# Kernel optimization log

Hardware: AMD Instinct MI355X
Metric: run time of the kernel (lower is better)

The kernel has to match this reference:

```python
import jax, jax.numpy as jnp
import numpy as np

B, S, IN_DIM = 128, 1024, 256
M, D, OUT = 64, 128, 128


def setup_inputs() -> dict:
    key = jax.random.key(0)
    ks = jax.random.split(key, 10)
    def xavier(k, shape):
        fan_in, fan_out = shape[-1], shape[-2] if len(shape) > 1 else shape[-1]
        lim = jnp.sqrt(6.0 / (shape[0] + shape[1]))
        return jax.random.uniform(k, shape, jnp.float32, -lim, lim)
    return {
        "x": jax.random.normal(ks[0], (B, S, IN_DIM), jnp.float32),
        "memory_key": xavier(ks[1], (M, D)),
        "memory_value": xavier(ks[2], (M, D)),
        "Wr": xavier(ks[3], (IN_DIM, D)),
        "br": jnp.zeros((D,), jnp.float32),
        "Ww": xavier(ks[4], (IN_DIM, D)),
        "bw": jnp.zeros((D,), jnp.float32),
        "Wp": xavier(ks[5], (D, OUT)),
        "bp": jnp.zeros((OUT,), jnp.float32),
    }


def reference(x, memory_key, memory_value, Wr, br, Ww, bw, Wp, bp):
    # Precompute time-parallel parts: read keys and write erase/add signals.
    k_all = jnp.einsum("bsi,id->bsd", x, Wr) + br          # [B,S,D]
    v_all = jnp.einsum("bsi,id->bsd", x, Ww) + bw          # [B,S,D]
    erase_all = jax.nn.sigmoid(v_all)                        # [B,S,D]
    add_all = jnp.tanh(v_all)                                # [B,S,D]

    Mv0 = jnp.broadcast_to(memory_value, (x.shape[0],) + memory_value.shape)  # [B,M,D]

    def step(Mv, inp):
        k_t, e_t, a_t = inp                                  # each [B,D]
        w = jax.nn.softmax(k_t @ memory_key.T, axis=-1)      # [B,M]
        r = jnp.einsum("bm,bmd->bd", w, Mv)                # [B,D]
        y = jax.nn.sigmoid(r @ Wp + bp)                      # [B,OUT]
        wE = w[:, :, None]                                   # [B,M,1]
        Mv = Mv * (1.0 - wE * e_t[:, None, :]) + wE * a_t[:, None, :]
        return Mv, y

    xs = (jnp.swapaxes(k_all, 0, 1),
          jnp.swapaxes(erase_all, 0, 1),
          jnp.swapaxes(add_all, 0, 1))                       # [S,B,D] each
    _, ys = jax.lax.scan(step, Mv0, xs)                      # ys: [S,B,OUT]
    return jnp.swapaxes(ys, 0, 1)                            # [B,S,OUT]
```

## Files before the change

### kernel.cpp

```cpp
#include <hip/hip_runtime.h>
#include <hip/hip_bf16.h>


#define B_   128
#define S_   1024
#define IN_  256
#define M_   64
#define D_   128
#define OUT_ 128
#define TC_  4
#define TL_  (S_ / TC_)
#define RC_  (B_ * TL_)

typedef __hip_bfloat16 bf16;
typedef unsigned int uint32;
typedef __attribute__((ext_vector_type(8))) short s16x8;
typedef __attribute__((ext_vector_type(4))) float f32x4;

__device__ __forceinline__ float tof(bf16 v) { return __bfloat162float(v); }
__device__ __forceinline__ bf16  tob(float v) { return __float2bfloat16(v); }
__device__ __forceinline__ float ldf(const float* p, long i) { return p[i]; }
__device__ __forceinline__ float ldf(const bf16* p, long i)  { return tof(p[i]); }
__device__ __forceinline__ void  stf(float* p, long i, float v) { p[i] = v; }
__device__ __forceinline__ void  stf(bf16* p, long i, float v)  { p[i] = tob(v); }
__device__ __forceinline__ void  unp(uint32 u, float& lo, float& hi) {
  lo = __uint_as_float(u << 16);
  hi = __uint_as_float(u & 0xFFFF0000u);
}
__device__ __forceinline__ uint32 pk(float lo, float hi) {
  union { bf16 h; unsigned short u; } a, b;
  a.h = tob(lo); b.h = tob(hi);
  return (uint32)a.u | ((uint32)b.u << 16);
}
__device__ __forceinline__ void split2(float f0, float f1, uint32& h, uint32& l) {
  union { bf16 b; unsigned short u; } a0, a1;
  a0.b = tob(f0); a1.b = tob(f1);
  h = (uint32)a0.u | ((uint32)a1.u << 16);
  const float r0 = f0 - tof(a0.b);
  const float r1 = f1 - tof(a1.b);
  l = pk(r0, r1);
}

__global__ __launch_bounds__(256) void k_probe(const uint32* __restrict__ xw,
                                               int* __restrict__ flag) {
  __shared__ int s[256];
  const int tid = threadIdx.x;
  int sc = 0;
#pragma unroll
  for (int k = 0; k < 8; ++k) {
    const uint32 u = xw[tid * 8 + k];
    const float v = __uint_as_float(u << 16);
    if (!(fabsf(v) < 4.0f)) sc++;
  }
  s[tid] = sc;
  __syncthreads();
  for (int o = 128; o > 0; o >>= 1) {
    if (tid < o) s[tid] += s[tid + o];
    __syncthreads();
  }
  if (tid == 0) *flag = (s[0] > 64) ? 1 : 0;
}

template <typename T>
__device__ void k0_body(const T* Wr, const T* br, const T* K,
                        float* Wk, float* bk) {
  const int idx = blockIdx.x * 256 + threadIdx.x;
  if (idx < IN_ * M_) {
    const int i = idx >> 6, m = idx & 63;
    float acc = 0.f;
    for (int d = 0; d < D_; ++d)
      acc = fmaf(ldf(Wr, (long)i * D_ + d), ldf(K, (long)m * D_ + d), acc);
    Wk[idx] = acc;
  } else if (idx < IN_ * M_ + M_) {
    const int m = idx - IN_ * M_;
    float acc = 0.f;
    for (int d = 0; d < D_; ++d)
      acc = fmaf(ldf(br, d), ldf(K, (long)m * D_ + d), acc);
    bk[m] = acc;
  }
}

__global__ __launch_bounds__(256) void k0_fold(const void* Wr, const void* br,
                                               const void* K, float* Wk, float* bk,
                                               const int* flag) {
  if (*flag) k0_body<float>((const float*)Wr, (const float*)br, (const float*)K, Wk, bk);
  else       k0_body<bf16>((const bf16*)Wr, (const bf16*)br, (const bf16*)K, Wk, bk);
}

__global__ __launch_bounds__(256) void k0b_pack(const void* Ww, const void* Wp,
                                                const float* Wk, bf16* WTh, bf16* WTl,
                                                bf16* WpTh, bf16* WpTl,
                                                const int* flag) {
  const int f = *flag;
  const int idx = blockIdx.x * 256 + threadIdx.x;
  if (f) {
    const float* Wwf = (const float*)Ww;
    const float* Wpf = (const float*)Wp;
    if (idx < 192 * 256) {
      const int n = idx >> 8, k = idx & 255;
      const float v = (n < 128) ? Wwf[k * 128 + n] : Wk[k * 64 + (n - 128)];
      const bf16 h = tob(v);
      WTh[idx] = h;
      WTl[idx] = tob(v - tof(h));
    } else {
      const int j = idx - 192 * 256;
      const int n = j >> 7, k = j & 127;
      const float v = Wpf[k * 128 + n];
      const bf16 h = tob(v);
      WpTh[j] = h;
      WpTl[j] = tob(v - tof(h));
    }
  } else {
    const bf16* Wwb = (const bf16*)Ww;
    const bf16* Wpb = (const bf16*)Wp;
    if (idx < 192 * 256) {
      const int n = idx >> 8, k = idx & 255;
      WTh[idx] = (n < 128) ? Wwb[k * 128 + n] : tob(Wk[k * 64 + (n - 128)]);
    } else {
      const int j = idx - 192 * 256;
      const int n = j >> 7, k = j & 127;
      WpTh[j] = Wpb[k * 128 + n];
    }
  }
}

template <bool F32>
__device__ void k1_body(const void* x, const void* bw, const float* bk,
                        const bf16* __restrict__ WTh, const bf16* __restrict__ WTl,
                        uint32* __restrict__ ea_all, bf16* __restrict__ w_all,
                        int chunk) {
  const int tid = threadIdx.x;
  const int wave = tid >> 6, lane = tid & 63;
  const int l15 = lane & 15, quad = lane >> 4;
  const int b = blockIdx.x >> 2, tb = blockIdx.x & 3;
  const int t0 = tb * 64 + wave * 16;
  const long lr0 = (long)b * TL_ + t0;
  const long ar0 = (long)b * S_ + (long)chunk * TL_ + t0;

  s16x8 afh[8], afl[8];
  if constexpr (F32) {
    const float* xr = (const float*)x + (ar0 + l15) * (long)IN_ + quad * 8;
#pragma unroll
    for (int k = 0; k < 8; ++k) {
      const float4 u0 = *(const float4*)(xr + k * 32);
      const float4 u1 = *(const float4*)(xr + k * 32 + 4);
      union { s16x8 v; uint32 u[4]; } H, L;
      split2(u0.x, u0.y, H.u[0], L.u[0]);
      split2(u0.z, u0.w, H.u[1], L.u[1]);
      split2(u1.x, u1.y, H.u[2], L.u[2]);
      split2(u1.z, u1.w, H.u[3], L.u[3]);
      afh[k] = H.v;
      afl[k] = L.v;
    }
  } else {
    const bf16* xr = (const bf16*)x + (ar0 + l15) * (long)IN_ + quad * 8;
#pragma unroll
    for (int k = 0; k < 8; ++k) afh[k] = *(const s16x8*)(xr + k * 32);
  }

  f32x4 acc[12];
#pragma unroll
  for (int ct = 0; ct < 12; ++ct) acc[ct] = (f32x4){0.f, 0.f, 0.f, 0.f};

#pragma unroll
  for (int ct = 0; ct < 12; ++ct) {
    const bf16* wph = WTh + ((ct * 16 + l15) << 8) + quad * 8;
    const bf16* wpl = WTl + ((ct * 16 + l15) << 8) + quad * 8;
#pragma unroll
    for (int k = 0; k < 8; ++k) {
      const s16x8 bh = *(const s16x8*)(wph + k * 32);
      acc[ct] = __builtin_amdgcn_mfma_f32_16x16x32_bf16(afh[k], bh, acc[ct], 0, 0, 0);
      if constexpr (F32) {
        const s16x8 bl = *(const s16x8*)(wpl + k * 32);
        acc[ct] = __builtin_amdgcn_mfma_f32_16x16x32_bf16(afl[k], bh, acc[ct], 0, 0, 0);
        acc[ct] = __builtin_amdgcn_mfma_f32_16x16x32_bf16(afh[k], bl, acc[ct], 0, 0, 0);
      }
    }
  }

#pragma unroll
  for (int ct = 0; ct < 8; ++ct) {
    const int col = ct * 16 + l15;
    float bb;
    if constexpr (F32) bb = ((const float*)bw)[col];
    else               bb = tof(((const bf16*)bw)[col]);
#pragma unroll
    for (int r = 0; r < 4; ++r) {
      const float v = acc[ct][r] + bb;
      const float sg = 1.0f / (1.0f + exp2f(-1.44269504f * v));
      const float th = 1.0f - 2.0f / (exp2f(2.88539008f * v) + 1.0f);
      ea_all[(lr0 + quad * 4 + r) * D_ + col] = pk(sg, th);
    }
  }
  float bks[4];
#pragma unroll
  for (int g = 0; g < 4; ++g) bks[g] = bk[g * 16 + l15];
#pragma unroll
  for (int r = 0; r < 4; ++r) {
    float s[4];
    float mx = -1e30f;
#pragma unroll
    for (int g = 0; g < 4; ++g) {
      s[g] = acc[8 + g][r] + bks[g];
      mx = fmaxf(mx, s[g]);
    }
#pragma unroll
    for (int off = 1; off < 16; off <<= 1) mx = fmaxf(mx, __shfl_xor(mx, off, 64));
    float ex[4], sum = 0.f;
#pragma unroll
    for (int g = 0; g < 4; ++g) {
      ex[g] = exp2f(1.44269504f * (s[g] - mx));
      sum += ex[g];
    }
#pragma unroll
    for (int off = 1; off < 16; off <<= 1) sum += __shfl_xor(sum, off, 64);
    const float inv = 1.0f / sum;
    const long lr = lr0 + quad * 4 + r;
#pragma unroll
    for (int g = 0; g < 4; ++g)
      w_all[lr * M_ + g * 16 + l15] = tob(ex[g] * inv);
  }
}

__global__ __launch_bounds__(256) void k1_mfma(const void* x, const void* bw,
                                               const float* bk, const bf16* WTh,
                                               const bf16* WTl, uint32* ea_all,
                                               bf16* w_all, int chunk,
                                               const int* __restrict__ flag) {
  if (*flag) k1_body<true>(x, bw, bk, WTh, WTl, ea_all, w_all, chunk);
  else       k1_body<false>(x, bw, bk, WTh, WTl, ea_all, w_all, chunk);
}

template <typename T>
__device__ void k2_body(const T* Mv0, const uint32* ea_all, const bf16* w_all,
                        float* MvS, T* r_out, int chunk) {
  const int tid = threadIdx.x;
  const int wave = tid >> 6, lane = tid & 63;
  const int mg = lane >> 2, dl = lane & 3;
  const int b = blockIdx.x & 127;
  const int dg = ((blockIdx.x >> 7) << 2) + wave;
  const int d = dg * 4 + dl;
  const int m0 = mg * 4;

  float Mv[4];
  if (chunk == 0) {
#pragma unroll
    for (int j = 0; j < 4; ++j)
      Mv[j] = ldf(Mv0, (long)(m0 + j) * D_ + d);
  } else {
#pragma unroll
    for (int j = 0; j < 4; ++j)
      Mv[j] = MvS[((long)b * M_ + m0 + j) * D_ + d];
  }

  const long lrbase = (long)b * TL_;
  const long arbase = (long)b * S_ + (long)chunk * TL_;
  const uint32* eap = ea_all + lrbase * D_ + d;
  const bf16* wap = w_all + lrbase * M_ + m0;

  uint32 erA[8], erB[8];
  uint2 wrA[8], wrB[8];
  float rbuf[8];
#pragma unroll
  for (int p = 0; p < 8; ++p) {
    erA[p] = eap[p * D_];
    wrA[p] = *(const uint2*)(wap + p * M_);
  }

  for (int t = 0; t < TL_; t += 16) {
#pragma unroll
    for (int p = 0; p < 8; ++p) {
      const int ln = t + 8 + p;
      erB[p] = eap[(long)ln * D_];
      wrB[p] = *(const uint2*)(wap + (long)ln * M_);
    }
#pragma unroll
    for (int p = 0; p < 8; ++p) {
      float e, a;
      unp(erA[p], e, a);
      float wv[4];
      unp(wrA[p].x, wv[0], wv[1]);
      unp(wrA[p].y, wv[2], wv[3]);
      float r = 0.f;
#pragma unroll
      for (int j = 0; j < 4; ++j) {
        const float c1 = fmaf(-wv[j], e, 1.0f);
        const float c2 = wv[j] * a;
        r = fmaf(wv[j], Mv[j], r);
        Mv[j] = fmaf(Mv[j], c1, c2);
      }
      r += __shfl_xor(r, 4, 64);
      r += __shfl_xor(r, 8, 64);
      r += __shfl_xor(r, 16, 64);
      r += __shfl_xor(r, 32, 64);
      rbuf[p] = r;
    }
    if (mg == 0) {
#pragma unroll
      for (int p = 0; p < 8; ++p)
        stf(r_out, (arbase + t + p) * D_ + d, rbuf[p]);
    }
#pragma unroll
    for (int p = 0; p < 8; ++p) {
      int ln = t + 16 + p;
      ln = ln < TL_ ? ln : TL_ - 1;
      erA[p] = eap[(long)ln * D_];
      wrA[p] = *(const uint2*)(wap + (long)ln * M_);
    }
#pragma unroll
    for (int p = 0; p < 8; ++p) {
      float e, a;
      unp(erB[p], e, a);
      float wv[4];
      unp(wrB[p].x, wv[0], wv[1]);
      unp(wrB[p].y, wv[2], wv[3]);
      float r = 0.f;
#pragma unroll
      for (int j = 0; j < 4; ++j) {
        const float c1 = fmaf(-wv[j], e, 1.0f);
        const float c2 = wv[j] * a;
        r = fmaf(wv[j], Mv[j], r);
        Mv[j] = fmaf(Mv[j], c1, c2);
      }
      r += __shfl_xor(r, 4, 64);
      r += __shfl_xor(r, 8, 64);
      r += __shfl_xor(r, 16, 64);
      r += __shfl_xor(r, 32, 64);
      rbuf[p] = r;
    }
    if (mg == 0) {
#pragma unroll
      for (int p = 0; p < 8; ++p)
        stf(r_out, (arbase + t + 8 + p) * D_ + d, rbuf[p]);
    }
  }
#pragma unroll
  for (int j = 0; j < 4; ++j)
    MvS[((long)b * M_ + m0 + j) * D_ + d] = Mv[j];
}

__global__ __launch_bounds__(256) void k2_scan(const void* Mv0, const uint32* ea_all,
                                               const bf16* w_all, float* MvS,
                                               void* r_out, int chunk,
                                               const int* flag) {
  if (*flag) k2_body<float>((const float*)Mv0, ea_all, w_all, MvS,
                            (float*)r_out, chunk);
  else       k2_body<bf16>((const bf16*)Mv0, ea_all, w_all, MvS,
                           (bf16*)r_out, chunk);
}

template <bool F32>
__device__ void k3_body(const bf16* __restrict__ WpTh, const bf16* __restrict__ WpTl,
                        const void* bpv, void* iov) {
  const int tid = threadIdx.x;
  const int wave = tid >> 6, lane = tid & 63;
  const int l15 = lane & 15, quad = lane >> 4;
  const long row0 = (long)blockIdx.x * 64 + wave * 16;

  s16x8 afh[4], afl[4];
  if constexpr (F32) {
    const float* rr = (const float*)iov + (row0 + l15) * D_ + quad * 8;
#pragma unroll
    for (int k = 0; k < 4; ++k) {
      const float4 u0 = *(const float4*)(rr + k * 32);
      const float4 u1 = *(const float4*)(rr + k * 32 + 4);
      union { s16x8 v; uint32 u[4]; } H, L;
      split2(u0.x, u0.y, H.u[0], L.u[0]);
      split2(u0.z, u0.w, H.u[1], L.u[1]);
      split2(u1.x, u1.y, H.u[2], L.u[2]);
      split2(u1.z, u1.w, H.u[3], L.u[3]);
      afh[k] = H.v;
      afl[k] = L.v;
    }
  } else {
    const bf16* rr = (const bf16*)iov + (row0 + l15) * D_ + quad * 8;
#pragma unroll
    for (int k = 0; k < 4; ++k) afh[k] = *(const s16x8*)(rr + k * 32);
  }

  f32x4 acc[8];
#pragma unroll
  for (int ct = 0; ct < 8; ++ct) acc[ct] = (f32x4){0.f, 0.f, 0.f, 0.f};
#pragma unroll
  for (int ct = 0; ct < 8; ++ct) {
    const bf16* wph = WpTh + ((ct * 16 + l15) << 7) + quad * 8;
    const bf16* wpl = WpTl + ((ct * 16 + l15) << 7) + quad * 8;
#pragma unroll
    for (int k = 0; k < 4; ++k) {
      const s16x8 bh = *(const s16x8*)(wph + k * 32);
      acc[ct] = __builtin_amdgcn_mfma_f32_16x16x32_bf16(afh[k], bh, acc[ct], 0, 0, 0);
      if constexpr (F32) {
        const s16x8 bl = *(const s16x8*)(wpl + k * 32);
        acc[ct] = __builtin_amdgcn_mfma_f32_16x16x32_bf16(afl[k], bh, acc[ct], 0, 0, 0);
        acc[ct] = __builtin_amdgcn_mfma_f32_16x16x32_bf16(afh[k], bl, acc[ct], 0, 0, 0);
      }
    }
  }
#pragma unroll
  for (int ct = 0; ct < 8; ++ct) {
    const int col = ct * 16 + l15;
    float bb;
    if constexpr (F32) bb = ((const float*)bpv)[col];
    else               bb = tof(((const bf16*)bpv)[col]);
#pragma unroll
    for (int r = 0; r < 4; ++r) {
      const float y = 1.0f / (1.0f + exp2f(-1.44269504f * (acc[ct][r] + bb)));
      if constexpr (F32)
        ((float*)iov)[(row0 + quad * 4 + r) * OUT_ + col] = y;
      else
        ((bf16*)iov)[(row0 + quad * 4 + r) * OUT_ + col] = tob(y);
    }
  }
}

__global__ __launch_bounds__(256) void k3_mfma(const bf16* __restrict__ WpTh,
                                               const bf16* __restrict__ WpTl,
                                               const void* bpv, void* iov,
                                               const int* __restrict__ flag) {
  if (*flag) k3_body<true>(WpTh, WpTl, bpv, iov);
  else       k3_body<false>(WpTh, WpTl, bpv, iov);
}

extern "C" void kernel_launch(void* const* d_in, const int* in_sizes, int n_in,
                              void* d_out, int out_size, void* d_ws, size_t ws_size,
                              hipStream_t stream) {
  const void* x   = d_in[0];
  const void* mk  = d_in[1];
  const void* mv  = d_in[2];
  const void* Wr  = d_in[3];
  const void* br  = d_in[4];
  const void* Ww  = d_in[5];
  const void* bwv = d_in[6];
  const void* Wp  = d_in[7];
  const void* bp  = d_in[8];

  char* ws = (char*)d_ws;
  int*    flag   = (int*)ws;
  float*  Wk     = (float*)(ws + 16);
  float*  bk     = (float*)(ws + 16 + 65536);
  bf16*   WTh    = (bf16*)(ws + 65808);
  bf16*   WTl    = WTh + 192 * 256;
  bf16*   WpTh   = WTl + 192 * 256;
  bf16*   WpTl   = WpTh + 128 * 128;
  uint32* ea_all = (uint32*)(WpTl + 128 * 128);
  bf16*   w_all  = (bf16*)(ea_all + (size_t)RC_ * D_);
  float*  MvS    = (float*)(w_all + (size_t)RC_ * M_);

  k_probe<<<1, 256, 0, stream>>>((const uint32*)x, flag);
  k0_fold<<<(IN_ * M_ + M_ + 255) / 256, 256, 0, stream>>>(Wr, br, mk, Wk, bk, flag);
  k0b_pack<<<256, 256, 0, stream>>>(Ww, Wp, Wk, WTh, WTl, WpTh, WpTl, flag);
  for (int c = 0; c < TC_; ++c) {
    k1_mfma<<<RC_ / 64, 256, 0, stream>>>(x, bwv, bk, WTh, WTl, ea_all, w_all, c, flag);
    k2_scan<<<B_ * 8, 256, 0, stream>>>(mv, ea_all, w_all, MvS, d_out, c, flag);
  }
  k3_mfma<<<(B_ * S_) / 64, 256, 0, stream>>>(WpTh, WpTl, bp, d_out, flag);
}
```

Measured before the change: 753.1 us.

## Choose scan chunk count from workspace size and simplify memory update FMA

The number of time chunks is now picked at runtime as the smallest power of two whose intermediate buffers fit in the workspace, instead of a fixed four chunks. With enough workspace this can mean a single k1/k2 pass with no state spill between launches. The per-step memory update is rewritten as Mv + w*(a - e*Mv), two FMAs instead of three ops, which shortens the serial dependency chain in the scan. The final state store is skipped on the last chunk. The risk is that larger chunks write bigger intermediates that may not stay in cache.

```diff
diff --git a/kernel.cpp b/kernel.cpp
--- a/kernel.cpp
+++ b/kernel.cpp
@@ -8,9 +8,7 @@
 #define M_   64
 #define D_   128
 #define OUT_ 128
-#define TC_  4
-#define TL_  (S_ / TC_)
-#define RC_  (B_ * TL_)
+#define NROWS_ (B_ * S_)
 
 typedef __hip_bfloat16 bf16;
 typedef unsigned int uint32;
@@ -128,14 +126,15 @@
 __device__ void k1_body(const void* x, const void* bw, const float* bk,
                         const bf16* __restrict__ WTh, const bf16* __restrict__ WTl,
                         uint32* __restrict__ ea_all, bf16* __restrict__ w_all,
-                        int chunk) {
+                        int chunk, int TL, int tshift) {
   const int tid = threadIdx.x;
   const int wave = tid >> 6, lane = tid & 63;
   const int l15 = lane & 15, quad = lane >> 4;
-  const int b = blockIdx.x >> 2, tb = blockIdx.x & 3;
+  const int b = blockIdx.x >> tshift;
+  const int tb = blockIdx.x & ((1 << tshift) - 1);
   const int t0 = tb * 64 + wave * 16;
-  const long lr0 = (long)b * TL_ + t0;
-  const long ar0 = (long)b * S_ + (long)chunk * TL_ + t0;
+  const long lr0 = (long)b * TL + t0;
+  const long ar0 = (long)b * S_ + (long)chunk * TL + t0;
 
   s16x8 afh[8], afl[8];
   if constexpr (F32) {
@@ -225,15 +224,16 @@
 __global__ __launch_bounds__(256) void k1_mfma(const void* x, const void* bw,
                                                const float* bk, const bf16* WTh,
                                                const bf16* WTl, uint32* ea_all,
-                                               bf16* w_all, int chunk,
+                                               bf16* w_all, int chunk, int TL,
+                                               int tshift,
                                                const int* __restrict__ flag) {
-  if (*flag) k1_body<true>(x, bw, bk, WTh, WTl, ea_all, w_all, chunk);
-  else       k1_body<false>(x, bw, bk, WTh, WTl, ea_all, w_all, chunk);
+  if (*flag) k1_body<true>(x, bw, bk, WTh, WTl, ea_all, w_all, chunk, TL, tshift);
+  else       k1_body<false>(x, bw, bk, WTh, WTl, ea_all, w_all, chunk, TL, tshift);
 }
 
 template <typename T>
 __device__ void k2_body(const T* Mv0, const uint32* ea_all, const bf16* w_all,
-                        float* MvS, T* r_out, int chunk) {
+                        float* MvS, T* r_out, int chunk, int TL, int TC) {
   const int tid = threadIdx.x;
   const int wave = tid >> 6, lane = tid & 63;
   const int mg = lane >> 2, dl = lane & 3;
@@ -253,8 +253,8 @@
       Mv[j] = MvS[((long)b * M_ + m0 + j) * D_ + d];
   }
 
-  const long lrbase = (long)b * TL_;
-  const long arbase = (long)b * S_ + (long)chunk * TL_;
+  const long lrbase = (long)b * TL;
+  const long arbase = (long)b * S_ + (long)chunk * TL;
   const uint32* eap = ea_all + lrbase * D_ + d;
   const bf16* wap = w_all + lrbase * M_ + m0;
 
@@ -267,7 +267,7 @@
     wrA[p] = *(const uint2*)(wap + p * M_);
   }
 
-  for (int t = 0; t < TL_; t += 16) {
+  for (int t = 0; t < TL; t += 16) {
 #pragma unroll
     for (int p = 0; p < 8; ++p) {
       const int ln = t + 8 + p;
@@ -284,10 +284,8 @@
       float r = 0.f;
 #pragma unroll
       for (int j = 0; j < 4; ++j) {
-        const float c1 = fmaf(-wv[j], e, 1.0f);
-        const float c2 = wv[j] * a;
         r = fmaf(wv[j], Mv[j], r);
-        Mv[j] = fmaf(Mv[j], c1, c2);
+        Mv[j] = fmaf(wv[j], fmaf(-e, Mv[j], a), Mv[j]);
       }
       r += __shfl_xor(r, 4, 64);
       r += __shfl_xor(r, 8, 64);
@@ -303,7 +301,7 @@
 #pragma unroll
     for (int p = 0; p < 8; ++p) {
       int ln = t + 16 + p;
-      ln = ln < TL_ ? ln : TL_ - 1;
+      ln = ln < TL ? ln : TL - 1;
       erA[p] = eap[(long)ln * D_];
       wrA[p] = *(const uint2*)(wap + (long)ln * M_);
     }
@@ -317,10 +315,8 @@
       float r = 0.f;
 #pragma unroll
       for (int j = 0; j < 4; ++j) {
-        const float c1 = fmaf(-wv[j], e, 1.0f);
-        const float c2 = wv[j] * a;
         r = fmaf(wv[j], Mv[j], r);
-        Mv[j] = fmaf(Mv[j], c1, c2);
+        Mv[j] = fmaf(wv[j], fmaf(-e, Mv[j], a), Mv[j]);
       }
       r += __shfl_xor(r, 4, 64);
       r += __shfl_xor(r, 8, 64);
@@ -334,19 +330,21 @@
         stf(r_out, (arbase + t + 8 + p) * D_ + d, rbuf[p]);
     }
   }
-#pragma unroll
-  for (int j = 0; j < 4; ++j)
-    MvS[((long)b * M_ + m0 + j) * D_ + d] = Mv[j];
+  if (chunk < TC - 1) {
+#pragma unroll
+    for (int j = 0; j < 4; ++j)
+      MvS[((long)b * M_ + m0 + j) * D_ + d] = Mv[j];
+  }
 }
 
 __global__ __launch_bounds__(256) void k2_scan(const void* Mv0, const uint32* ea_all,
                                                const bf16* w_all, float* MvS,
-                                               void* r_out, int chunk,
-                                               const int* flag) {
+                                               void* r_out, int chunk, int TL,
+                                               int TC, const int* flag) {
   if (*flag) k2_body<float>((const float*)Mv0, ea_all, w_all, MvS,
-                            (float*)r_out, chunk);
+                            (float*)r_out, chunk, TL, TC);
   else       k2_body<bf16>((const bf16*)Mv0, ea_all, w_all, MvS,
-                           (bf16*)r_out, chunk);
+                           (bf16*)r_out, chunk, TL, TC);
 }
 
 template <bool F32>
@@ -435,23 +433,39 @@
   const void* bp  = d_in[8];
 
   char* ws = (char*)d_ws;
-  int*    flag   = (int*)ws;
-  float*  Wk     = (float*)(ws + 16);
-  float*  bk     = (float*)(ws + 16 + 65536);
-  bf16*   WTh    = (bf16*)(ws + 65808);
-  bf16*   WTl    = WTh + 192 * 256;
-  bf16*   WpTh   = WTl + 192 * 256;
-  bf16*   WpTl   = WpTh + 128 * 128;
-  uint32* ea_all = (uint32*)(WpTl + 128 * 128);
-  bf16*   w_all  = (bf16*)(ea_all + (size_t)RC_ * D_);
-  float*  MvS    = (float*)(w_all + (size_t)RC_ * M_);
+  int*    flag = (int*)ws;
+  float*  Wk   = (float*)(ws + 16);
+  float*  bk   = (float*)(ws + 16 + 65536);
+  bf16*   WTh  = (bf16*)(ws + 65808);
+  bf16*   WTl  = WTh + 192 * 256;
+  bf16*   WpTh = WTl + 192 * 256;
+  bf16*   WpTl = WpTh + 128 * 128;
+  char*   dyn  = (char*)(WpTl + 128 * 128);
+  const size_t fixed = (size_t)(dyn - ws);
+
+  int TC = 16;
+  for (int c = 1; c <= 16; c <<= 1) {
+    const size_t rc = (size_t)NROWS_ / c;
+    const size_t need = fixed + rc * (D_ * 4 + M_ * 2) +
+                        (c > 1 ? (size_t)B_ * M_ * D_ * 4 : 0) + 1024;
+    if (need <= ws_size) { TC = c; break; }
+  }
+  const int TL = S_ / TC;
+  const int tshift = __builtin_ctz(TL / 64);
+  const size_t RC = (size_t)NROWS_ / TC;
+
+  uint32* ea_all = (uint32*)dyn;
+  bf16*   w_all  = (bf16*)(ea_all + RC * D_);
+  float*  MvS    = (float*)(w_all + RC * M_);
 
   k_probe<<<1, 256, 0, stream>>>((const uint32*)x, flag);
   k0_fold<<<(IN_ * M_ + M_ + 255) / 256, 256, 0, stream>>>(Wr, br, mk, Wk, bk, flag);
   k0b_pack<<<256, 256, 0, stream>>>(Ww, Wp, Wk, WTh, WTl, WpTh, WpTl, flag);
-  for (int c = 0; c < TC_; ++c) {
-    k1_mfma<<<RC_ / 64, 256, 0, stream>>>(x, bwv, bk, WTh, WTl, ea_all, w_all, c, flag);
-    k2_scan<<<B_ * 8, 256, 0, stream>>>(mv, ea_all, w_all, MvS, d_out, c, flag);
-  }
-  k3_mfma<<<(B_ * S_) / 64, 256, 0, stream>>>(WpTh, WpTl, bp, d_out, flag);
-}
+  for (int c = 0; c < TC; ++c) {
+    k1_mfma<<<(int)(RC / 64), 256, 0, stream>>>(x, bwv, bk, WTh, WTl, ea_all, w_all,
+                                                c, TL, tshift, flag);
+    k2_scan<<<B_ * 8, 256, 0, stream>>>(mv, ea_all, w_all, MvS, d_out, c, TL, TC,
+                                        flag);
+  }
+  k3_mfma<<<NROWS_ / 64, 256, 0, stream>>>(WpTh, WpTl, bp, d_out, flag);
+}
```

After: 699.7 us. 7.1% less time.
